# Optimization experiments

Hardware: AMD Instinct MI355X
Metric: run time of the kernel (lower is better)

Reference implementation:

```python
import jax, jax.numpy as jnp
import numpy as np

H = W = 28  # fixed grid size hardcoded in the module
ATOL = 1e-8  # torch.allclose(v, 0.0) default tolerance


def setup_inputs() -> dict:
    key = jax.random.key(0)
    k1, k2, k3 = jax.random.split(key, 3)
    B = 32768
    x = jax.random.normal(k1, (B, 1, H, W), dtype=jnp.float32)
    # pos2d: integer grid (as in reset_parameters) plus small learned jitter
    g0, g1 = jnp.meshgrid(jnp.arange(H, dtype=jnp.float32),
                          jnp.arange(W, dtype=jnp.float32), indexing='ij')
    grid = jnp.stack([g0, g1], axis=-1)  # [28,28,2]
    pos2d = grid + 0.5 * jax.random.normal(k2, (H, W, 2), dtype=jnp.float32)
    # weight: around the 0.167 init value
    weight = 0.167 + 0.05 * jax.random.uniform(k3, (H, W), dtype=jnp.float32)
    return {"input": x, "pos2d": pos2d, "weight": weight}


def reference(input, pos2d, weight):
    # input: [B,1,28,28]; pos2d: [28,28,2]; weight: [28,28]
    x = input[:, 0]                       # [B,28,28]
    sw = jax.nn.relu(weight)              # [28,28]
    ce = jnp.round(pos2d)                 # rounded centers, [28,28,2]
    acc = jnp.zeros_like(x)
    # fixed 5x5 deformable neighborhood (25 structurally distinct offsets)
    for i0 in range(-2, 3):
        for i1 in range(-2, 3):
            off = jnp.array([i0, i1], dtype=pos2d.dtype)
            cr = ce + off                 # neighbor coords (float, integer-valued)
            cri = cr.astype(jnp.int32)
            in_b = ((cri[..., 0] >= 0) & (cri[..., 0] < H) &
                    (cri[..., 1] >= 0) & (cri[..., 1] < W))  # [28,28]
            idx0 = jnp.clip(cri[..., 0], 0, H - 1)
            idx1 = jnp.clip(cri[..., 1], 0, W - 1)
            v = x[:, idx0, idx1]          # [B,28,28] gather (same idx per batch)
            v = jnp.where(in_b[None], v, 0.0)
            # torch.allclose(v, 0.0) short-circuit: tiny values treated as 0
            v = jnp.where(jnp.abs(v) <= ATOL, 0.0, v)
            dis = cr - pos2d              # distance to learned center
            w = jnp.exp(-0.5 * jnp.sum(dis * dis, axis=-1))  # [28,28]
            acc = acc + v * w[None]
    out = acc * sw[None]
    return out[:, None]                   # [B,1,28,28]
```

## Files before the change

### kernel.cpp

```cpp
#include <hip/hip_runtime.h>

#define HH 28
#define WW 28
#define NPIX 784
#define BLOCK 832

__global__ __launch_bounds__(BLOCK, 1) void axs_89807766159734_kernel(
    const float* __restrict__ x, const float* __restrict__ pos2d,
    const float* __restrict__ weight, float* __restrict__ out,
    int nGroups)
{
    __shared__ float4 lds[NPIX];
    const int p = threadIdx.x;
    const bool act = p < NPIX;

    float coef[25];
    int   boff[25];
    if (act) {
        const float p0 = pos2d[2*p],   p1 = pos2d[2*p + 1];
        const float sw = fmaxf(weight[p], 0.0f);
        const float ce0 = rintf(p0), ce1 = rintf(p1);
#pragma unroll
        for (int t = 0; t < 25; ++t) {
            const int i0 = t / 5 - 2, i1 = t % 5 - 2;
            const float cr0 = ce0 + (float)i0, cr1 = ce1 + (float)i1;
            const int c0 = (int)cr0, c1 = (int)cr1;
            const bool inb = (c0 >= 0) & (c0 < HH) & (c1 >= 0) & (c1 < WW);
            const int q0 = min(max(c0, 0), HH - 1);
            const int q1 = min(max(c1, 0), WW - 1);
            const float d0 = cr0 - p0, d1 = cr1 - p1;
            const float w = __expf(-0.5f * (d0*d0 + d1*d1));
            coef[t] = inb ? sw * w : 0.0f;
            boff[t] = (q0 * WW + q1) * 16;
        }
    }

    int g = blockIdx.x;
    float v0 = 0.f, v1 = 0.f, v2 = 0.f, v3 = 0.f;
    if (g < nGroups && act) {
        const size_t base = (size_t)g * 4u * NPIX;
        v0 = x[base + p];
        v1 = x[base + NPIX + p];
        v2 = x[base + 2*NPIX + p];
        v3 = x[base + 3*NPIX + p];
    }

    for (; g < nGroups; g += gridDim.x) {
        __syncthreads();
        if (act) lds[p] = make_float4(v0, v1, v2, v3);
        __syncthreads();

        const int gn = g + gridDim.x;
        if (gn < nGroups && act) {
            const size_t nb = (size_t)gn * 4u * NPIX;
            v0 = x[nb + p];
            v1 = x[nb + NPIX + p];
            v2 = x[nb + 2*NPIX + p];
            v3 = x[nb + 3*NPIX + p];
        }

        if (act) {
            float a0 = 0.f, a1 = 0.f, a2 = 0.f, a3 = 0.f;
#pragma unroll
            for (int t = 0; t < 25; ++t) {
                const float4 v = *(const float4*)((const char*)lds + boff[t]);
                const float c = coef[t];
                a0 = fmaf(c, v.x, a0);
                a1 = fmaf(c, v.y, a1);
                a2 = fmaf(c, v.z, a2);
                a3 = fmaf(c, v.w, a3);
            }
            const size_t base = (size_t)g * 4u * NPIX;
            out[base + p]          = a0;
            out[base + NPIX + p]   = a1;
            out[base + 2*NPIX + p] = a2;
            out[base + 3*NPIX + p] = a3;
        }
    }
}

extern "C" void kernel_launch(void* const* d_in, const int* in_sizes, int n_in,
                              void* d_out, int out_size, void* d_ws, size_t ws_size,
                              hipStream_t stream) {
    const float* x      = (const float*)d_in[0];
    const float* pos2d  = (const float*)d_in[1];
    const float* weight = (const float*)d_in[2];
    float* out = (float*)d_out;

    const int B = in_sizes[0] / NPIX;
    const int nGroups = B / 4;
    int blocks = nGroups < 1024 ? nGroups : 1024;

    hipLaunchKernelGGL(axs_89807766159734_kernel, dim3(blocks), dim3(BLOCK), 0, stream,
                       x, pos2d, weight, out, nGroups);
}
```

Measured before the change: 194.1 us.

## Process 32 images per block with swizzled LDS tile and fp16 coefficient table

Each block now stages 32 images (8 float4 columns per pixel) in LDS instead of 4. It uses an XOR swizzle on the column index to spread bank accesses, and a persistent grid of 256 blocks with register prefetch of the next group. Per-pixel coefficients move from registers into a shared fp16 table, and the rounded centers into a shared short table. Gather indices are recomputed per task. This is meant to raise the amount of work per block and cut register pressure. It uses about 143KB of LDS, so likely one block per CU. Storing coefficients in fp16 adds rounding error, and the strided global access pattern (8 images interleaved per wavefront) may coalesce poorly.

```diff
diff --git a/kernel.cpp b/kernel.cpp
--- a/kernel.cpp
+++ b/kernel.cpp
@@ -1,80 +1,104 @@
 #include <hip/hip_runtime.h>
+#include <hip/hip_fp16.h>
 
 #define HH 28
 #define WW 28
 #define NPIX 784
-#define BLOCK 832
+#define NIMG 32
+#define BLOCK 768
+#define NTASK (NPIX * 8)
+#define MAXT 9
 
-__global__ __launch_bounds__(BLOCK, 1) void axs_89807766159734_kernel(
+__global__ __launch_bounds__(BLOCK, 3) void axs_89807766159734_kernel(
     const float* __restrict__ x, const float* __restrict__ pos2d,
-    const float* __restrict__ weight, float* __restrict__ out,
-    int nGroups)
+    const float* __restrict__ weight, float* __restrict__ out, int nGroups)
 {
-    __shared__ float4 lds[NPIX];
-    const int p = threadIdx.x;
-    const bool act = p < NPIX;
+    __shared__ float4 buf[NTASK];
+    __shared__ __half ctab[NPIX][26];
+    __shared__ short  sce0[NPIX], sce1[NPIX];
 
-    float coef[25];
-    int   boff[25];
-    if (act) {
-        const float p0 = pos2d[2*p],   p1 = pos2d[2*p + 1];
-        const float sw = fmaxf(weight[p], 0.0f);
+    const int tid = threadIdx.x;
+
+    for (int p = tid; p < NPIX; p += BLOCK) {
+        const float p0 = pos2d[2*p], p1 = pos2d[2*p+1];
+        const float sw = fmaxf(weight[p], 0.f);
         const float ce0 = rintf(p0), ce1 = rintf(p1);
+        sce0[p] = (short)(int)ce0;
+        sce1[p] = (short)(int)ce1;
 #pragma unroll
         for (int t = 0; t < 25; ++t) {
-            const int i0 = t / 5 - 2, i1 = t % 5 - 2;
+            const int i0 = t/5 - 2, i1 = t%5 - 2;
             const float cr0 = ce0 + (float)i0, cr1 = ce1 + (float)i1;
             const int c0 = (int)cr0, c1 = (int)cr1;
-            const bool inb = (c0 >= 0) & (c0 < HH) & (c1 >= 0) & (c1 < WW);
-            const int q0 = min(max(c0, 0), HH - 1);
-            const int q1 = min(max(c1, 0), WW - 1);
-            const float d0 = cr0 - p0, d1 = cr1 - p1;
-            const float w = __expf(-0.5f * (d0*d0 + d1*d1));
-            coef[t] = inb ? sw * w : 0.0f;
-            boff[t] = (q0 * WW + q1) * 16;
+            const bool inb = (c0>=0)&(c0<HH)&(c1>=0)&(c1<WW);
+            const float d0 = cr0-p0, d1 = cr1-p1;
+            const float w = __expf(-0.5f*(d0*d0+d1*d1));
+            ctab[p][t] = __float2half(inb ? sw*w : 0.f);
         }
+        ctab[p][25] = __float2half(0.f);
     }
 
     int g = blockIdx.x;
-    float v0 = 0.f, v1 = 0.f, v2 = 0.f, v3 = 0.f;
-    if (g < nGroups && act) {
-        const size_t base = (size_t)g * 4u * NPIX;
-        v0 = x[base + p];
-        v1 = x[base + NPIX + p];
-        v2 = x[base + 2*NPIX + p];
-        v3 = x[base + 3*NPIX + p];
+    float4 pre[MAXT];
+    if (g < nGroups) {
+        int k = 0;
+        for (int s = tid; s < NTASK; s += BLOCK, ++k) {
+            const int q = s >> 3, c = s & 7;
+            const int ib = (g*NIMG + 4*c)*NPIX + q;
+            pre[k] = make_float4(x[ib], x[ib+NPIX], x[ib+2*NPIX], x[ib+3*NPIX]);
+        }
     }
 
     for (; g < nGroups; g += gridDim.x) {
         __syncthreads();
-        if (act) lds[p] = make_float4(v0, v1, v2, v3);
+        {
+            int k = 0;
+            for (int s = tid; s < NTASK; s += BLOCK, ++k) {
+                const int q = s >> 3, c = s & 7;
+                buf[q*8 + (c ^ (q & 7))] = pre[k];
+            }
+        }
         __syncthreads();
 
         const int gn = g + gridDim.x;
-        if (gn < nGroups && act) {
-            const size_t nb = (size_t)gn * 4u * NPIX;
-            v0 = x[nb + p];
-            v1 = x[nb + NPIX + p];
-            v2 = x[nb + 2*NPIX + p];
-            v3 = x[nb + 3*NPIX + p];
+        if (gn < nGroups) {
+            int k = 0;
+            for (int s = tid; s < NTASK; s += BLOCK, ++k) {
+                const int q = s >> 3, c = s & 7;
+                const int ib = (gn*NIMG + 4*c)*NPIX + q;
+                pre[k] = make_float4(x[ib], x[ib+NPIX], x[ib+2*NPIX], x[ib+3*NPIX]);
+            }
         }
 
-        if (act) {
-            float a0 = 0.f, a1 = 0.f, a2 = 0.f, a3 = 0.f;
+        for (int tau = tid; tau < NTASK; tau += BLOCK) {
+            const int p = tau >> 3, c = tau & 7;
+            const int e0 = sce0[p], e1 = sce1[p];
+            uint cw[13];
+            {
+                const uint* crow = (const uint*)&ctab[p][0];
+#pragma unroll
+                for (int j = 0; j < 13; ++j) cw[j] = crow[j];
+            }
+            float4 acc = make_float4(0.f,0.f,0.f,0.f);
 #pragma unroll
             for (int t = 0; t < 25; ++t) {
-                const float4 v = *(const float4*)((const char*)lds + boff[t]);
-                const float c = coef[t];
-                a0 = fmaf(c, v.x, a0);
-                a1 = fmaf(c, v.y, a1);
-                a2 = fmaf(c, v.z, a2);
-                a3 = fmaf(c, v.w, a3);
+                const int i0 = t/5 - 2, i1 = t%5 - 2;
+                int c0 = e0 + i0; c0 = min(max(c0,0), HH-1);
+                int c1 = e1 + i1; c1 = min(max(c1,0), WW-1);
+                const int q = c0*WW + c1;
+                const float4 v = buf[q*8 + (c ^ (q & 7))];
+                const __half2 h2 = *(const __half2*)&cw[t>>1];
+                const float coef = __half2float((t&1) ? __high2half(h2) : __low2half(h2));
+                acc.x = fmaf(coef, v.x, acc.x);
+                acc.y = fmaf(coef, v.y, acc.y);
+                acc.z = fmaf(coef, v.z, acc.z);
+                acc.w = fmaf(coef, v.w, acc.w);
             }
-            const size_t base = (size_t)g * 4u * NPIX;
-            out[base + p]          = a0;
-            out[base + NPIX + p]   = a1;
-            out[base + 2*NPIX + p] = a2;
-            out[base + 3*NPIX + p] = a3;
+            const int ob = (g*NIMG + 4*c)*NPIX + p;
+            out[ob]        = acc.x;
+            out[ob+NPIX]   = acc.y;
+            out[ob+2*NPIX] = acc.z;
+            out[ob+3*NPIX] = acc.w;
         }
     }
 }
@@ -88,8 +112,8 @@
     float* out = (float*)d_out;
 
     const int B = in_sizes[0] / NPIX;
-    const int nGroups = B / 4;
-    int blocks = nGroups < 1024 ? nGroups : 1024;
+    const int nGroups = B / NIMG;
+    const int blocks = 256;
 
     hipLaunchKernelGGL(axs_89807766159734_kernel, dim3(blocks), dim3(BLOCK), 0, stream,
                        x, pos2d, weight, out, nGroups);
```

New measurement: 252.5 us. 1.3x slower.

## Recast 5x5 deformable stencil as banded fp16 MFMA GEMM over batch tiles

Applied to the files above, without the earlier changes.

Replaces per-pixel 25-tap gather FMA loop with a banded matrix formulation: each block owns a 112-pixel strip, precomputes fp16 coefficient fragments over a 12-row K band, stages 64-image batch tiles in LDS as fp16, and multiplies with 16x16x32 f16 MFMA. Grid is split into strips and batch chunks. This trades exact fp32 math for fp16 inputs, rereads each input image once per strip, and drops the tiny-value zeroing, risking tolerance and extra memory traffic.

```diff
diff --git a/kernel.cpp b/kernel.cpp
--- a/kernel.cpp
+++ b/kernel.cpp
@@ -1,80 +1,111 @@
 #include <hip/hip_runtime.h>
 
-#define HH 28
-#define WW 28
-#define NPIX 784
-#define BLOCK 832
+#define HHH   28
+#define NPIX  784
+#define NSTRIP 7
+#define M_PIX 112
+#define KBAND 336
+#define NKT   11
+#define XPITCH 360
+#define NB    64
+#define NNT   4
+#define BLOCK 448
+#define CHUNKS 74
 
-__global__ __launch_bounds__(BLOCK, 1) void axs_89807766159734_kernel(
+typedef _Float16 half8  __attribute__((ext_vector_type(8)));
+typedef _Float16 half4h __attribute__((ext_vector_type(4)));
+typedef float    floatx4 __attribute__((ext_vector_type(4)));
+
+__global__ __launch_bounds__(BLOCK, 4) void axs_89807766159734_kernel(
     const float* __restrict__ x, const float* __restrict__ pos2d,
     const float* __restrict__ weight, float* __restrict__ out,
-    int nGroups)
+    int tilesPerChunk, int totalTiles)
 {
-    __shared__ float4 lds[NPIX];
-    const int p = threadIdx.x;
-    const bool act = p < NPIX;
+    __shared__ _Float16 X16[NB * XPITCH];
+    __shared__ int s_rlo;
 
-    float coef[25];
-    int   boff[25];
-    if (act) {
-        const float p0 = pos2d[2*p],   p1 = pos2d[2*p + 1];
-        const float sw = fmaxf(weight[p], 0.0f);
-        const float ce0 = rintf(p0), ce1 = rintf(p1);
+    const int strip = blockIdx.x;
+    const int chunk = blockIdx.y;
+    const int tid  = threadIdx.x;
+    const int lane = tid & 63;
+    const int w    = tid >> 6;
+    const int ml   = lane & 15;
+    const int g    = lane >> 4;
+
+    const int p_glob = strip * M_PIX + w * 16 + ml;
+    const float p0 = pos2d[2 * p_glob];
+    const float p1 = pos2d[2 * p_glob + 1];
+    const float sw = fmaxf(weight[p_glob], 0.f);
+    const float ce0f = rintf(p0);
+    const int ce0 = (int)ce0f, ce1 = (int)rintf(p1);
+
+    if (tid == 0) s_rlo = 1 << 30;
+    __syncthreads();
+    if (lane < 16) atomicMin(&s_rlo, ce0 - 2);
+    __syncthreads();
+    const int r_lo = s_rlo;
+
+    half8 af[NKT];
 #pragma unroll
-        for (int t = 0; t < 25; ++t) {
-            const int i0 = t / 5 - 2, i1 = t % 5 - 2;
-            const float cr0 = ce0 + (float)i0, cr1 = ce1 + (float)i1;
-            const int c0 = (int)cr0, c1 = (int)cr1;
-            const bool inb = (c0 >= 0) & (c0 < HH) & (c1 >= 0) & (c1 < WW);
-            const int q0 = min(max(c0, 0), HH - 1);
-            const int q1 = min(max(c1, 0), WW - 1);
-            const float d0 = cr0 - p0, d1 = cr1 - p1;
-            const float w = __expf(-0.5f * (d0*d0 + d1*d1));
-            coef[t] = inb ? sw * w : 0.0f;
-            boff[t] = (q0 * WW + q1) * 16;
+    for (int Kt = 0; Kt < NKT; ++Kt) {
+#pragma unroll
+        for (int j = 0; j < 8; ++j) {
+            const int k = Kt * 32 + g * 8 + j;
+            const int qr = (int)(((unsigned)k * 2341u) >> 16);
+            const int qc = k - 28 * qr;
+            const int qrow = r_lo + qr;
+            const int i0 = qrow - ce0, i1 = qc - ce1;
+            float coef = 0.f;
+            if (i0 >= -2 && i0 <= 2 && i1 >= -2 && i1 <= 2 &&
+                qrow >= 0 && qrow < HHH && k < KBAND) {
+                const float d0 = (float)qrow - p0, d1 = (float)qc - p1;
+                coef = sw * __expf(-0.5f * (d0 * d0 + d1 * d1));
+            }
+            af[Kt][j] = (_Float16)coef;
         }
     }
 
-    int g = blockIdx.x;
-    float v0 = 0.f, v1 = 0.f, v2 = 0.f, v3 = 0.f;
-    if (g < nGroups && act) {
-        const size_t base = (size_t)g * 4u * NPIX;
-        v0 = x[base + p];
-        v1 = x[base + NPIX + p];
-        v2 = x[base + 2*NPIX + p];
-        v3 = x[base + 3*NPIX + p];
-    }
+    const int k_lo = max(0, -r_lo * 28);
+    const int k_hi = min(KBAND, (HHH - r_lo) * 28);
+    const int tile0 = chunk * tilesPerChunk;
 
-    for (; g < nGroups; g += gridDim.x) {
+    for (int t = 0; t < tilesPerChunk; ++t) {
+        const int tile = tile0 + t;
+        if (tile >= totalTiles) break;
+        const int bbase = tile * NB;
+
         __syncthreads();
-        if (act) lds[p] = make_float4(v0, v1, v2, v3);
+        for (int e = tid; e < NB * (XPITCH / 4); e += BLOCK) {
+            const int b  = e / (XPITCH / 4);
+            const int k0 = (e - b * (XPITCH / 4)) * 4;
+            const float* src = x + (size_t)(bbase + b) * NPIX + r_lo * 28;
+            half4h h;
+#pragma unroll
+            for (int j = 0; j < 4; ++j) {
+                const int k = k0 + j;
+                h[j] = (_Float16)((k >= k_lo && k < k_hi) ? src[k] : 0.f);
+            }
+            *(half4h*)&X16[b * XPITCH + k0] = h;
+        }
         __syncthreads();
 
-        const int gn = g + gridDim.x;
-        if (gn < nGroups && act) {
-            const size_t nb = (size_t)gn * 4u * NPIX;
-            v0 = x[nb + p];
-            v1 = x[nb + NPIX + p];
-            v2 = x[nb + 2*NPIX + p];
-            v3 = x[nb + 3*NPIX + p];
+        floatx4 acc[NNT];
+#pragma unroll
+        for (int Nt = 0; Nt < NNT; ++Nt) acc[Nt] = (floatx4){0.f, 0.f, 0.f, 0.f};
+#pragma unroll
+        for (int Kt = 0; Kt < NKT; ++Kt) {
+#pragma unroll
+            for (int Nt = 0; Nt < NNT; ++Nt) {
+                const half8 bf = *(const half8*)&X16[(Nt * 16 + ml) * XPITCH + Kt * 32 + g * 8];
+                acc[Nt] = __builtin_amdgcn_mfma_f32_16x16x32_f16(af[Kt], bf, acc[Nt], 0, 0, 0);
+            }
         }
 
-        if (act) {
-            float a0 = 0.f, a1 = 0.f, a2 = 0.f, a3 = 0.f;
+        const int pg = strip * M_PIX + w * 16 + g * 4;
 #pragma unroll
-            for (int t = 0; t < 25; ++t) {
-                const float4 v = *(const float4*)((const char*)lds + boff[t]);
-                const float c = coef[t];
-                a0 = fmaf(c, v.x, a0);
-                a1 = fmaf(c, v.y, a1);
-                a2 = fmaf(c, v.z, a2);
-                a3 = fmaf(c, v.w, a3);
-            }
-            const size_t base = (size_t)g * 4u * NPIX;
-            out[base + p]          = a0;
-            out[base + NPIX + p]   = a1;
-            out[base + 2*NPIX + p] = a2;
-            out[base + 3*NPIX + p] = a3;
+        for (int Nt = 0; Nt < NNT; ++Nt) {
+            const int bg = bbase + Nt * 16 + ml;
+            *(floatx4*)&out[(size_t)bg * NPIX + pg] = acc[Nt];
         }
     }
 }
@@ -88,9 +119,9 @@
     float* out = (float*)d_out;
 
     const int B = in_sizes[0] / NPIX;
-    const int nGroups = B / 4;
-    int blocks = nGroups < 1024 ? nGroups : 1024;
+    const int totalTiles = B / NB;
+    const int tilesPerChunk = (totalTiles + CHUNKS - 1) / CHUNKS;
 
-    hipLaunchKernelGGL(axs_89807766159734_kernel, dim3(blocks), dim3(BLOCK), 0, stream,
-                       x, pos2d, weight, out, nGroups);
+    hipLaunchKernelGGL(axs_89807766159734_kernel, dim3(NSTRIP, CHUNKS), dim3(BLOCK), 0, stream,
+                       x, pos2d, weight, out, tilesPerChunk, totalTiles);
 }
```

Result: slower. 305.6 us (+57.5%).
